# Optimization experiments

Measured on AMD Instinct MI355X. Metric: run time of the kernel, lower is better.

The kernel has to match this reference:

```python
import jax, jax.numpy as jnp
import numpy as np

B, N, D, H, L, K, V = 2, 2048, 512, 8, 4, 32, 256
HD = D // H
MOD = 4294967296.0
SCALE = 1.0 / np.sqrt(HD)


def _ln(x, g, b):
    m = x.mean(-1, keepdims=True)
    v = ((x - m) ** 2).mean(-1, keepdims=True)
    return (x - m) * jax.lax.rsqrt(v + 1e-5) * g + b


def _expmap0(v, c):
    sc = jnp.sqrt(c)
    vn = jnp.maximum(jnp.linalg.norm(v, axis=-1, keepdims=True), 1e-8)
    return jnp.tanh(sc * vn) * v / (sc * vn)


def _knn_poincare(pos, c):
    xx = jnp.sum(pos ** 2, -1)                                    # [N]
    d2 = jnp.maximum(xx[:, None] + xx[None, :] - 2.0 * pos @ pos.T, 0.0)
    denom = (1.0 - c * xx)[:, None] * (1.0 - c * xx)[None, :] + 1e-8
    arg = jnp.maximum(1.0 + 2.0 * c * d2 / denom, 1.0)
    dist = jnp.arccosh(arg) / jnp.sqrt(c)                         # [N,N]
    neg_d, idx = jax.lax.top_k(-dist, K)                          # smallest-k
    return -neg_d, idx                                            # [N,K],[N,K]


def _forward(hashes, indices, emb, hash_proj, Wb, bb, log_c, pos_tangent,
             Wq, bq, Wk, bk, Wv, bv, Wo, bo, W1, b1, W2, b2,
             g1, be1, g2, be2, log_tau, Wout, bout):
    c = jnp.exp(log_c)
    char = emb[indices]                                           # [B,N,D]
    he = (hashes[..., None].astype(jnp.float32) / MOD) @ hash_proj  # [B,N,D]
    x = jnp.concatenate([char, he], -1) @ Wb + bb                 # [B,N,D]

    # kNN structure computed under no_grad in the original
    pos = _expmap0(jax.lax.stop_gradient(pos_tangent), jax.lax.stop_gradient(c))
    attn_dists, idx = _knn_poincare(pos, jax.lax.stop_gradient(c))  # shared over batch

    for i in range(L):
        xn = _ln(x, g1[i], be1[i])
        q = (xn @ Wq[i] + bq[i]).reshape(B, N, H, HD).transpose(0, 2, 1, 3)
        k = (xn @ Wk[i] + bk[i]).reshape(B, N, H, HD).transpose(0, 2, 1, 3)
        v = (xn @ Wv[i] + bv[i]).reshape(B, N, H, HD).transpose(0, 2, 1, 3)
        kg = k[:, :, idx, :]                                      # [B,H,N,K,HD]
        vg = v[:, :, idx, :]
        fs = jnp.einsum('bhnd,bhnkd->bhnk', q, kg) * SCALE
        gs = -attn_dists[None, None] / (jnp.exp(log_tau[i]) + 1e-8)
        p = jax.nn.softmax(fs + gs, axis=-1)                      # [B,H,N,K]
        ao = jnp.einsum('bhnk,bhnkd->bhnd', p, vg)
        ao = ao.transpose(0, 2, 1, 3).reshape(B, N, D)
        x = x + ao @ Wo[i] + bo[i]
        xn2 = _ln(x, g2[i], be2[i])
        x = x + jax.nn.gelu(xn2 @ W1[i] + b1[i], approximate=False) @ W2[i] + b2[i]

    return x[:, -1, :] @ Wout + bout                              # [B,V]


def setup_inputs():
    key = jax.random.key(0)
    ks = jax.random.split(key, 20)
    rn = lambda k, s, sc=0.02: jax.random.normal(k, s, jnp.float32) * sc
    z = lambda s: jnp.zeros(s, jnp.float32)
    o = lambda s: jnp.ones(s, jnp.float32)
    return {
        'hashes': jax.random.randint(ks[0], (B, N), 0, 1000000),
        'indices': jax.random.randint(ks[1], (B, N), 0, V),
        'emb': rn(ks[2], (V, D)),
        'hash_proj': rn(ks[3], (1, D)),
        'Wb': rn(ks[4], (2 * D, D)),
        'bb': z((D,)),
        'log_c': jnp.array(0.0, jnp.float32),
        'pos_tangent': rn(ks[5], (N, D)),
        'Wq': rn(ks[6], (L, D, D)), 'bq': z((L, D)),
        'Wk': rn(ks[7], (L, D, D)), 'bk': z((L, D)),
        'Wv': rn(ks[8], (L, D, D)), 'bv': z((L, D)),
        'Wo': rn(ks[9], (L, D, D)), 'bo': z((L, D)),
        'W1': rn(ks[10], (L, D, 4 * D)), 'b1': z((L, 4 * D)),
        'W2': rn(ks[11], (L, 4 * D, D)), 'b2': z((L, D)),
        'g1': o((L, D)), 'be1': z((L, D)),
        'g2': o((L, D)), 'be2': z((L, D)),
        'log_tau': z((L,)),
        'Wout': rn(ks[12], (D, V)), 'bout': z((V,)),
    }


def reference(hashes, indices, emb, hash_proj, Wb, bb, log_c, pos_tangent,
              Wq, bq, Wk, bk, Wv, bv, Wo, bo, W1, b1, W2, b2,
              g1, be1, g2, be2, log_tau, Wout, bout):
    return _forward(hashes, indices, emb, hash_proj, Wb, bb, log_c, pos_tangent,
                    Wq, bq, Wk, bk, Wv, bv, Wo, bo, W1, b1, W2, b2,
                    g1, be1, g2, be2, log_tau, Wout, bout)
```

## Files before the change

### kernel.cpp

```cpp
#include <hip/hip_runtime.h>
#include <hip/hip_bf16.h>
#include <math.h>

#define Bb 2
#define Nn 2048
#define Dd 512
#define Hh 8
#define Ll 4
#define Kk 32
#define Vv 256
#define HDh 64
#define Mrows (Bb*Nn)

static constexpr float SCALE_QK = 0.125f;
static constexpr float INV_MOD = 1.0f / 4294967296.0f;

typedef _Float16 f16;
typedef _Float16 f16x8 __attribute__((ext_vector_type(8)));
typedef _Float16 f16x4 __attribute__((ext_vector_type(4)));
typedef _Float16 f16x2 __attribute__((ext_vector_type(2)));
typedef float f32x4 __attribute__((ext_vector_type(4)));
typedef unsigned long long u64;

__global__ void scal_kernel(const float* __restrict__ log_c,
                            const float* __restrict__ log_tau,
                            float* __restrict__ scal) {
    int t = threadIdx.x;
    if (t == 0) {
        float c = expf(log_c[0]);
        scal[0] = c;
        scal[1] = sqrtf(c);
    }
    if (t < Ll) scal[2 + t] = 1.0f / (expf(log_tau[t]) + 1e-8f);
}

__global__ __launch_bounds__(256)
void hvec_part_kernel(const float* __restrict__ hash_proj,
                      const float* __restrict__ Wb,
                      float* __restrict__ part) {
    const int b = blockIdx.x;
    const int t = threadIdx.x;
    float a0 = 0.f, a1 = 0.f;
#pragma unroll
    for (int i = 0; i < 16; i++) {
        int kx = b * 16 + i;
        float hp = hash_proj[kx];
        const float* wr = Wb + (size_t)(Dd + kx) * Dd;
        a0 = fmaf(hp, wr[t], a0);
        a1 = fmaf(hp, wr[t + 256], a1);
    }
    part[b * Dd + t]       = a0;
    part[b * Dd + t + 256] = a1;
}
__global__ __launch_bounds__(256)
void hvec_red_kernel(const float* __restrict__ part, float* __restrict__ hvec) {
    const int n = blockIdx.x * 256 + threadIdx.x;
    float acc = 0.f;
#pragma unroll
    for (int b = 0; b < 32; b++) acc += part[b * Dd + n];
    hvec[n] = acc;
}

__global__ void conv_kernel(const float* __restrict__ src, f16* __restrict__ dst, int n) {
    int i = blockIdx.x * 256 + threadIdx.x;
    if (i < n) dst[i] = (f16)src[i];
}

__global__ void pack_bias_kernel(const float* __restrict__ bq, const float* __restrict__ bk,
                                 const float* __restrict__ bv, float* __restrict__ bqkv) {
    int t = blockIdx.x * 256 + threadIdx.x;
    int l = t / 1536, r = t % 1536;
    const float* src = (r < 512) ? bq : ((r < 1024) ? bk : bv);
    bqkv[t] = src[l * 512 + (r & 511)];
}

__global__ __launch_bounds__(256)
void trans_kernel(const float* __restrict__ src, f16* __restrict__ dst,
                  int K, int N, long sStride, long dStride) {
    __shared__ float tile[32][33];
    const float* s = src + blockIdx.z * sStride;
    f16* d = dst + blockIdx.z * dStride;
    int k0 = blockIdx.y * 32, n0 = blockIdx.x * 32;
    int tx = threadIdx.x & 31, ty = threadIdx.x >> 5;
#pragma unroll
    for (int i = 0; i < 32; i += 8)
        tile[ty + i][tx] = s[(long)(k0 + ty + i) * N + n0 + tx];
    __syncthreads();
#pragma unroll
    for (int i = 0; i < 32; i += 8)
        d[(long)(n0 + ty + i) * K + k0 + tx] = (f16)tile[tx][ty + i];
}

__global__ __launch_bounds__(256)
void trans4_kernel(const float* __restrict__ Wq, const float* __restrict__ Wk,
                   const float* __restrict__ Wv, const float* __restrict__ Wo,
                   f16* __restrict__ Wqkvt, f16* __restrict__ Wot) {
    __shared__ float tile[32][33];
    const int which = blockIdx.z >> 2, l = blockIdx.z & 3;
    const float* s;
    f16* d;
    switch (which) {
        case 0: s = Wq + (size_t)l * 262144; d = Wqkvt + (size_t)l * 786432;          break;
        case 1: s = Wk + (size_t)l * 262144; d = Wqkvt + (size_t)l * 786432 + 262144; break;
        case 2: s = Wv + (size_t)l * 262144; d = Wqkvt + (size_t)l * 786432 + 524288; break;
        default:s = Wo + (size_t)l * 262144; d = Wot   + (size_t)l * 262144;          break;
    }
    int k0 = blockIdx.y * 32, n0 = blockIdx.x * 32;
    int tx = threadIdx.x & 31, ty = threadIdx.x >> 5;
#pragma unroll
    for (int i = 0; i < 32; i += 8)
        tile[ty + i][tx] = s[(long)(k0 + ty + i) * 512 + n0 + tx];
    __syncthreads();
#pragma unroll
    for (int i = 0; i < 32; i += 8)
        d[(long)(n0 + ty + i) * 512 + k0 + tx] = (f16)tile[tx][ty + i];
}

template<int TN, bool GATHER, bool RANK1, bool GELU, bool RES, bool OUT16>
__global__ __launch_bounds__(256)
void mgemm(const f16* __restrict__ A, const f16* __restrict__ Wt,
           const float* __restrict__ bias,
           const int* __restrict__ gidx,
           const int* __restrict__ hashes, const float* __restrict__ hvec,
           const float* __restrict__ resid,
           void* __restrict__ Cout, int M, int N, int K) {
    constexpr int TM  = 64;
    constexpr int WRN = (TN == 64) ? 2 : 1;
    constexpr int WCN = 4 / WRN;
    constexpr int WRE = TM / WRN;
    constexpr int NIT = WRE / 16;
    constexpr int ACH = TM * 8;
    constexpr int BCH = TN * 8;
    constexpr int NCH = ACH + BCH;
    constexpr int NCHT = NCH / 256;
    __shared__ __align__(16) f16 sm[NCH * 8];
    const int t = threadIdx.x;
    const int lane = t & 63;
    const int w = t >> 6;
    const int wr = w / WCN, wc = w % WCN;
    const int i0 = blockIdx.y * TM, j0 = blockIdx.x * TN;

    const f16* gsrc[NCHT];
#pragma unroll
    for (int q = 0; q < NCHT; q++) {
        int c = t + q * 256;
        if (c < ACH) {
            int m = c >> 3, kb = (c & 7) ^ (m & 7);
            long row = GATHER ? (long)gidx[i0 + m] : (long)(i0 + m);
            gsrc[q] = A + row * K + kb * 8;
        } else {
            int cc = c - ACH;
            int n = cc >> 3, kb = (cc & 7) ^ (n & 7);
            gsrc[q] = Wt + (long)(j0 + n) * K + kb * 8;
        }
    }

    f32x4 acc[NIT][2];
#pragma unroll
    for (int i = 0; i < NIT; i++)
#pragma unroll
        for (int j = 0; j < 2; j++) acc[i][j] = (f32x4){0.f, 0.f, 0.f, 0.f};

    for (int kt = 0; kt < K; kt += 64) {
        f16x8 stg[NCHT];
#pragma unroll
        for (int q = 0; q < NCHT; q++) stg[q] = *(const f16x8*)(gsrc[q] + kt);
        __syncthreads();
#pragma unroll
        for (int q = 0; q < NCHT; q++)
            *(f16x8*)(sm + (t + q * 256) * 8) = stg[q];
        __syncthreads();

#pragma unroll
        for (int kh = 0; kh < 2; kh++) {
            f16x8 af[NIT], bf[2];
#pragma unroll
            for (int i = 0; i < NIT; i++) {
                int m = wr * WRE + i * 16 + (lane & 15);
                int sl = m * 8 + ((kh * 4 + (lane >> 4)) ^ (m & 7));
                af[i] = *(const f16x8*)(sm + sl * 8);
            }
#pragma unroll
            for (int j = 0; j < 2; j++) {
                int n = wc * 32 + j * 16 + (lane & 15);
                int sl = ACH + n * 8 + ((kh * 4 + (lane >> 4)) ^ (n & 7));
                bf[j] = *(const f16x8*)(sm + sl * 8);
            }
#pragma unroll
            for (int i = 0; i < NIT; i++)
#pragma unroll
                for (int j = 0; j < 2; j++)
                    acc[i][j] = __builtin_amdgcn_mfma_f32_16x16x32_f16(af[i], bf[j], acc[i][j], 0, 0, 0);
        }
    }

    float* Cf = (float*)Cout;
    f16*   Ch = (f16*)Cout;
#pragma unroll
    for (int i = 0; i < NIT; i++) {
        int rbase = i0 + wr * WRE + i * 16 + ((lane >> 4) << 2);
#pragma unroll
        for (int v = 0; v < 4; v++) {
            int row = rbase + v;
            float hterm = RANK1 ? (float)hashes[row] * INV_MOD : 0.f;
#pragma unroll
            for (int j = 0; j < 2; j++) {
                int col = j0 + wc * 32 + j * 16 + (lane & 15);
                float val = acc[i][j][v] + bias[col];
                if (RANK1) val += hterm * hvec[col];
                if (GELU)  val = 0.5f * val * (1.f + erff(val * 0.7071067811865475f));
                if (RES)   val += resid[(long)row * N + col];
                if (OUT16) Ch[(long)row * N + col] = (f16)val;
                else       Cf[(long)row * N + col] = val;
            }
        }
    }
}

__global__ __launch_bounds__(256)
void mdist_kernel(const f16* __restrict__ poshl, const float* __restrict__ xx,
                  const float* __restrict__ scal, float* __restrict__ dist) {
    constexpr int TM = 64, TN = 64;
    constexpr int ACH = TM * 8, BCH = TN * 8, NCH = ACH + BCH;
    constexpr int NCHT = NCH / 256;
    constexpr int KK = 1024;
    __shared__ __align__(16) f16 sm[NCH * 8];
    const int t = threadIdx.x;
    const int lane = t & 63;
    const int w = t >> 6;
    const int wr = w >> 1, wc = w & 1;
    const int i0 = blockIdx.y * TM, j0 = blockIdx.x * TN;

    const f16* gsrc[NCHT];
#pragma unroll
    for (int q = 0; q < NCHT; q++) {
        int c = t + q * 256;
        if (c < ACH) {
            int m = c >> 3, kb = (c & 7) ^ (m & 7);
            gsrc[q] = poshl + (long)(i0 + m) * KK + kb * 8;
        } else {
            int cc = c - ACH;
            int n = cc >> 3, kb = (cc & 7) ^ (n & 7);
            gsrc[q] = poshl + (long)(j0 + n) * KK + kb * 8;
        }
    }

    f32x4 acc[2][2];
#pragma unroll
    for (int i = 0; i < 2; i++)
#pragma unroll
        for (int j = 0; j < 2; j++) acc[i][j] = (f32x4){0.f, 0.f, 0.f, 0.f};

    for (int kt = 0; kt < KK; kt += 64) {
        f16x8 stg[NCHT];
#pragma unroll
        for (int q = 0; q < NCHT; q++) stg[q] = *(const f16x8*)(gsrc[q] + kt);
        __syncthreads();
#pragma unroll
        for (int q = 0; q < NCHT; q++)
            *(f16x8*)(sm + (t + q * 256) * 8) = stg[q];
        __syncthreads();

#pragma unroll
        for (int kh = 0; kh < 2; kh++) {
            f16x8 af[2], bf[2];
#pragma unroll
            for (int i = 0; i < 2; i++) {
                int m = wr * 32 + i * 16 + (lane & 15);
                int sl = m * 8 + ((kh * 4 + (lane >> 4)) ^ (m & 7));
                af[i] = *(const f16x8*)(sm + sl * 8);
            }
#pragma unroll
            for (int j = 0; j < 2; j++) {
                int n = wc * 32 + j * 16 + (lane & 15);
                int sl = ACH + n * 8 + ((kh * 4 + (lane >> 4)) ^ (n & 7));
                bf[j] = *(const f16x8*)(sm + sl * 8);
            }
#pragma unroll
            for (int i = 0; i < 2; i++)
#pragma unroll
                for (int j = 0; j < 2; j++)
                    acc[i][j] = __builtin_amdgcn_mfma_f32_16x16x32_f16(af[i], bf[j], acc[i][j], 0, 0, 0);
        }
    }

    const float c = scal[0];
#pragma unroll
    for (int i = 0; i < 2; i++) {
        int rbase = i0 + wr * 32 + i * 16 + ((lane >> 4) << 2);
#pragma unroll
        for (int v = 0; v < 4; v++) {
            int row = rbase + v;
            float xi = xx[row];
#pragma unroll
            for (int j = 0; j < 2; j++) {
                int col = j0 + wc * 32 + j * 16 + (lane & 15);
                float xj = xx[col];
                float d2 = fmaxf(xi + xj - 2.f * acc[i][j][v], 0.f);
                float denom = (1.f - c * xi) * (1.f - c * xj) + 1e-8f;
                float arg = fmaxf(1.f + 2.f * c * d2 / denom, 1.f);
                dist[(long)row * Nn + col] = arg;
            }
        }
    }
}

__global__ __launch_bounds__(64)
void ln_kernel(const float* __restrict__ x, const float* __restrict__ g,
               const float* __restrict__ be, f16* __restrict__ xn) {
    const int row = blockIdx.x, t = threadIdx.x;
    const float4* xr = (const float4*)(x + (size_t)row * Dd);
    float4 v0 = xr[t], v1 = xr[t + 64];
    float s = v0.x + v0.y + v0.z + v0.w + v1.x + v1.y + v1.z + v1.w;
#pragma unroll
    for (int off = 32; off; off >>= 1) s += __shfl_xor(s, off, 64);
    float mean = s * (1.f / Dd);
    float d0x = v0.x - mean, d0y = v0.y - mean, d0z = v0.z - mean, d0w = v0.w - mean;
    float d1x = v1.x - mean, d1y = v1.y - mean, d1z = v1.z - mean, d1w = v1.w - mean;
    float q = d0x*d0x + d0y*d0y + d0z*d0z + d0w*d0w
            + d1x*d1x + d1y*d1y + d1z*d1z + d1w*d1w;
#pragma unroll
    for (int off = 32; off; off >>= 1) q += __shfl_xor(q, off, 64);
    float rstd = rsqrtf(q * (1.f / Dd) + 1e-5f);
    float4 g0 = ((const float4*)g)[t], g1v = ((const float4*)g)[t + 64];
    float4 b0 = ((const float4*)be)[t], b1v = ((const float4*)be)[t + 64];
    f16* xo = xn + (size_t)row * Dd;
    f16x4 o0, o1;
    o0[0] = (f16)(d0x * rstd * g0.x + b0.x);
    o0[1] = (f16)(d0y * rstd * g0.y + b0.y);
    o0[2] = (f16)(d0z * rstd * g0.z + b0.z);
    o0[3] = (f16)(d0w * rstd * g0.w + b0.w);
    o1[0] = (f16)(d1x * rstd * g1v.x + b1v.x);
    o1[1] = (f16)(d1y * rstd * g1v.y + b1v.y);
    o1[2] = (f16)(d1z * rstd * g1v.z + b1v.z);
    o1[3] = (f16)(d1w * rstd * g1v.w + b1v.w);
    *(f16x4*)(xo + t * 4)         = o0;
    *(f16x4*)(xo + (t + 64) * 4)  = o1;
}

__global__ __launch_bounds__(256)
void expmap_kernel(const float* __restrict__ vt, const float* __restrict__ scal,
                   f16* __restrict__ poshl, float* __restrict__ xx) {
    __shared__ float red[256];
    const int row = blockIdx.x, t = threadIdx.x;
    const float* vr = vt + (size_t)row * Dd;
    float v0 = vr[t], v1 = vr[t + 256];
    red[t] = v0 * v0 + v1 * v1;
    __syncthreads();
    for (int off = 128; off; off >>= 1) {
        if (t < off) red[t] += red[t + off];
        __syncthreads();
    }
    float total = red[0];
    float vn = fmaxf(sqrtf(total), 1e-8f);
    float sc = scal[1];
    float factor = tanhf(sc * vn) / (sc * vn);
    float p0 = factor * v0, p1 = factor * v1;
    f16 h0 = (f16)p0, h1 = (f16)p1;
    f16* pr = poshl + (size_t)row * 1024;
    pr[t]             = h0;
    pr[t + 256]       = h1;
    pr[512 + t]       = (f16)(p0 - (float)h0);
    pr[512 + t + 256] = (f16)(p1 - (float)h1);
    if (t == 0) xx[row] = factor * factor * total;
}

__global__ __launch_bounds__(256)
void topk_kernel(const float* __restrict__ dist, const float* __restrict__ scal,
                 float* __restrict__ outd, int* __restrict__ outi) {
    __shared__ unsigned wred[4];
    __shared__ unsigned bc;
    __shared__ __align__(8) u64 buf[128];
    const int t = threadIdx.x;
    const int w = t >> 6;
    const int n = blockIdx.x;
    const float sqc = scal[1];
    const uint4* dr = (const uint4*)(dist + (size_t)n * Nn);

    uint4 va = dr[t * 2];
    uint4 vb = dr[t * 2 + 1];
    unsigned k[8] = {va.x, va.y, va.z, va.w, vb.x, vb.y, vb.z, vb.w};
    const int g0 = t * 8;

    unsigned lo = 0x3F800000u;
    unsigned hi = 0x7F800001u;
    unsigned chi = 2048u;
    while (chi > 96u && (hi - lo) > 1u) {
        unsigned mid = lo + ((hi - lo) >> 1);
        int c = 0;
#pragma unroll
        for (int j = 0; j < 8; j++) c += (k[j] < mid) ? 1 : 0;
#pragma unroll
        for (int off = 32; off; off >>= 1) c += __shfl_xor(c, off, 64);
        __syncthreads();
        if ((t & 63) == 0) wred[w] = (unsigned)c;
        __syncthreads();
        unsigned ct = wred[0] + wred[1] + wred[2] + wred[3];
        if (ct >= 32u) { hi = mid; chi = ct; } else { lo = mid; }
    }

    if (chi <= 96u) {
        if (t == 0) bc = 0u;
        __syncthreads();
#pragma unroll
        for (int j = 0; j < 8; j++) {
            if (k[j] < hi) {
                unsigned s = atomicAdd(&bc, 1u);
                buf[s] = ((u64)k[j] << 11) | (u64)(unsigned)(g0 + j);
            }
        }
        __syncthreads();
        const int m = (int)chi;
        if (t < m) {
            u64 my = buf[t];
            int r = 0;
            for (int j = 0; j < m; j++) r += (buf[j] < my) ? 1 : 0;
            if (r < Kk) {
                float v = __uint_as_float((unsigned)(my >> 11));
                outd[n * Kk + r] = acoshf(v) / sqc;
                outi[n * Kk + r] = (int)(my & 2047u);
            }
        }
    } else {
        int c = 0;
#pragma unroll
        for (int j = 0; j < 8; j++) c += (k[j] < lo) ? 1 : 0;
#pragma unroll
        for (int off = 32; off; off >>= 1) c += __shfl_xor(c, off, 64);
        __syncthreads();
        if ((t & 63) == 0) wred[w] = (unsigned)c;
        if (t == 0) bc = 0u;
        __syncthreads();
        const int cless = (int)(wred[0] + wred[1] + wred[2] + wred[3]);
#pragma unroll
        for (int j = 0; j < 8; j++) {
            if (k[j] < lo) {
                unsigned s = atomicAdd(&bc, 1u);
                buf[s] = ((u64)k[j] << 11) | (u64)(unsigned)(g0 + j);
            }
        }
        __syncthreads();
        if (t < cless) {
            u64 my = buf[t];
            int r = 0;
            for (int j = 0; j < cless; j++) r += (buf[j] < my) ? 1 : 0;
            float v = __uint_as_float((unsigned)(my >> 11));
            outd[n * Kk + r] = acoshf(v) / sqc;
            outi[n * Kk + r] = (int)(my & 2047u);
        }
        const int need = Kk - cless;
        unsigned eqm = 0u;
#pragma unroll
        for (int j = 0; j < 8; j++) if (k[j] == lo) eqm |= (1u << j);
        const float dv = acoshf(__uint_as_float(lo)) / sqc;
        for (int s = 0; s < need; s++) {
            int mi = 0x7FFFFFFF;
#pragma unroll
            for (int j = 0; j < 8; j++)
                if (eqm & (1u << j)) mi = min(mi, g0 + j);
#pragma unroll
            for (int off = 32; off; off >>= 1) mi = min(mi, __shfl_xor(mi, off, 64));
            __syncthreads();
            if ((t & 63) == 0) wred[w] = (unsigned)mi;
            __syncthreads();
            int m4 = (int)min(min(wred[0], wred[1]), min(wred[2], wred[3]));
            int j = m4 - g0;
            if (j >= 0 && j < 8 && (eqm & (1u << j))) {
                eqm &= ~(1u << j);
                outd[n * Kk + cless + s] = dv;
                outi[n * Kk + cless + s] = m4;
            }
        }
    }
}

#define KVSTR 520
__global__ __launch_bounds__(256)
void attn_kernel(const f16* __restrict__ qkv, const float* __restrict__ adist,
                 const int* __restrict__ aidx, const float* __restrict__ scal,
                 int layer, f16* __restrict__ ao) {
    __shared__ __align__(16) f16 kv[64 * KVSTR];
    __shared__ __align__(16) f16 qs[512];
    __shared__ float ps[Hh][Kk];
    __shared__ float sdist[Kk];
    __shared__ int   sidx[Kk];
    const int t = threadIdx.x;
    const int b = blockIdx.x >> 11, n = blockIdx.x & (Nn - 1);
    const float inv_tau = scal[2 + layer];

    if (t < Kk) {
        sidx[t]  = aidx[n * Kk + t];
        sdist[t] = adist[n * Kk + t];
    }
    __syncthreads();

    {
        const size_t qrow = (size_t)(b * Nn + n) * 1536;
#pragma unroll
        for (int q = 0; q < 16; q++) {
            int c = q * 256 + t;
            int j = c >> 7, ci = c & 127;
            size_t src = (size_t)(b * Nn + sidx[j]) * 1536 + 512 + ci * 8;
            int dst = (ci < 64) ? (j * KVSTR + ci * 8)
                                : ((32 + j) * KVSTR + (ci - 64) * 8);
            *(f16x8*)(kv + dst) = *(const f16x8*)(qkv + src);
        }
        if (t < 64) *(f16x8*)(qs + t * 8) = *(const f16x8*)(qkv + qrow + t * 8);
    }
    __syncthreads();

    const int h = t >> 5, j = t & 31;
    float dot = 0.f;
#pragma unroll
    for (int i = 0; i < 8; i++) {
        f16x8 qa = *(const f16x8*)(qs + h * HDh + i * 8);
        f16x8 ka = *(const f16x8*)(kv + j * KVSTR + h * HDh + i * 8);
#pragma unroll
        for (int m = 0; m < 4; m++) {
            f16x2 qp = {qa[2 * m], qa[2 * m + 1]};
            f16x2 kp = {ka[2 * m], ka[2 * m + 1]};
            dot = __builtin_amdgcn_fdot2(qp, kp, dot, false);
        }
    }
    float s = dot * SCALE_QK - sdist[j] * inv_tau;
    float mx = s;
#pragma unroll
    for (int off = 16; off; off >>= 1) mx = fmaxf(mx, __shfl_xor(mx, off, 64));
    float e = expf(s - mx);
    float sum = e;
#pragma unroll
    for (int off = 16; off; off >>= 1) sum += __shfl_xor(sum, off, 64);
    ps[h][j] = e / sum;
    __syncthreads();

    const int d2 = t & 31;
    float a0 = 0.f, a1 = 0.f;
#pragma unroll
    for (int jj = 0; jj < Kk; jj++) {
        float p = ps[h][jj];
        f16x2 vv = *(const f16x2*)(kv + (32 + jj) * KVSTR + h * HDh + d2 * 2);
        a0 = fmaf(p, (float)vv[0], a0);
        a1 = fmaf(p, (float)vv[1], a1);
    }
    f16x2 outv; outv[0] = (f16)a0; outv[1] = (f16)a1;
    *(f16x2*)(ao + (size_t)(b * Nn + n) * Dd + h * HDh + d2 * 2) = outv;
}

__global__ void out_kernel(const float* __restrict__ x, const float* __restrict__ Wout,
                           const float* __restrict__ bout, float* __restrict__ out) {
    const int b = blockIdx.x, vc = threadIdx.x;
    const float* xr = x + ((size_t)(b * Nn + (Nn - 1))) * Dd;
    float acc = bout[vc];
    for (int d = 0; d < Dd; d++) acc = fmaf(xr[d], Wout[(size_t)d * Vv + vc], acc);
    out[b * Vv + vc] = acc;
}

static constexpr size_t X_OFF     = 0;
static constexpr size_t XN16_OFF  = 8388608;
static constexpr size_t QKV16_OFF = 12582912;
static constexpr size_t AO16_OFF  = 25165824;
static constexpr size_t H1_OFF    = 29360128;
static constexpr size_t AD_OFF    = 46137344;
static constexpr size_t AI_OFF    = 46399488;
static constexpr size_t SC_OFF    = 46661632;
static constexpr size_t HV_OFF    = 46661888;
static constexpr size_t XX_OFF    = 46663936;
static constexpr size_t BQKV_OFF  = 46672128;
static constexpr size_t EMB16_OFF = 46704896;
static constexpr size_t WBT_OFF   = 46967040;
static constexpr size_t WQKVT_OFF = 47491328;
static constexpr size_t WOT_OFF   = 53782784;
static constexpr size_t W1T_OFF   = 55879936;
static constexpr size_t W2T_OFF   = 64268544;
static constexpr size_t HP_OFF    = 72657152;

extern "C" void kernel_launch(void* const* d_in, const int* in_sizes, int n_in,
                              void* d_out, int out_size, void* d_ws, size_t ws_size,
                              hipStream_t stream) {
    (void)in_sizes; (void)n_in; (void)out_size; (void)ws_size;
    const int*   hashes    = (const int*)  d_in[0];
    const int*   indices   = (const int*)  d_in[1];
    const float* emb       = (const float*)d_in[2];
    const float* hash_proj = (const float*)d_in[3];
    const float* Wb        = (const float*)d_in[4];
    const float* bb        = (const float*)d_in[5];
    const float* log_c     = (const float*)d_in[6];
    const float* pos_t     = (const float*)d_in[7];
    const float* Wq        = (const float*)d_in[8];
    const float* bq        = (const float*)d_in[9];
    const float* Wk        = (const float*)d_in[10];
    const float* bk        = (const float*)d_in[11];
    const float* Wv        = (const float*)d_in[12];
    const float* bv        = (const float*)d_in[13];
    const float* Wo        = (const float*)d_in[14];
    const float* bo        = (const float*)d_in[15];
    const float* W1        = (const float*)d_in[16];
    const float* b1        = (const float*)d_in[17];
    const float* W2        = (const float*)d_in[18];
    const float* b2        = (const float*)d_in[19];
    const float* g1        = (const float*)d_in[20];
    const float* be1       = (const float*)d_in[21];
    const float* g2        = (const float*)d_in[22];
    const float* be2       = (const float*)d_in[23];
    const float* log_tau   = (const float*)d_in[24];
    const float* Wout      = (const float*)d_in[25];
    const float* bout      = (const float*)d_in[26];

    char* ws = (char*)d_ws;
    float* x      = (float*)(ws + X_OFF);
    f16*   xn16   = (f16*)  (ws + XN16_OFF);
    f16*   qkv16  = (f16*)  (ws + QKV16_OFF);
    f16*   ao16   = (f16*)  (ws + AO16_OFF);
    f16*   h1     = (f16*)  (ws + H1_OFF);
    float* adist  = (float*)(ws + AD_OFF);
    int*   aidx   = (int*)  (ws + AI_OFF);
    float* scal   = (float*)(ws + SC_OFF);
    float* hvec   = (float*)(ws + HV_OFF);
    float* xxb    = (float*)(ws + XX_OFF);
    float* bqkv   = (float*)(ws + BQKV_OFF);
    f16*   emb16  = (f16*)  (ws + EMB16_OFF);
    f16*   Wbt    = (f16*)  (ws + WBT_OFF);
    f16*   Wqkvt  = (f16*)  (ws + WQKVT_OFF);
    f16*   Wot    = (f16*)  (ws + WOT_OFF);
    f16*   W1t    = (f16*)  (ws + W1T_OFF);
    f16*   W2t    = (f16*)  (ws + W2T_OFF);
    float* hpart  = (float*)(ws + HP_OFF);
    f16*   poshl  = (f16*)  (ws + AO16_OFF);
    float* distb  = (float*)(ws + H1_OFF);

    scal_kernel<<<1, 64, 0, stream>>>(log_c, log_tau, scal);
    hvec_part_kernel<<<32, 256, 0, stream>>>(hash_proj, Wb, hpart);
    hvec_red_kernel<<<2, 256, 0, stream>>>(hpart, hvec);
    pack_bias_kernel<<<24, 256, 0, stream>>>(bq, bk, bv, bqkv);
    conv_kernel<<<(Vv * Dd + 255) / 256, 256, 0, stream>>>(emb, emb16, Vv * Dd);
    trans_kernel<<<dim3(16, 16, 1), 256, 0, stream>>>(Wb, Wbt, 512, 512, 0, 0);
    trans4_kernel<<<dim3(16, 16, 16), 256, 0, stream>>>(Wq, Wk, Wv, Wo, Wqkvt, Wot);
    trans_kernel<<<dim3(64, 16, Ll), 256, 0, stream>>>(W1, W1t, 512, 2048, 1048576, 1048576);
    trans_kernel<<<dim3(16, 64, Ll), 256, 0, stream>>>(W2, W2t, 2048, 512, 1048576, 1048576);

    mgemm<64, true, true, false, false, false><<<dim3(8, 64), 256, 0, stream>>>(
        emb16, Wbt, bb, indices, hashes, hvec, nullptr, x, Mrows, Dd, Dd);

    expmap_kernel<<<Nn, 256, 0, stream>>>(pos_t, scal, poshl, xxb);
    mdist_kernel<<<dim3(32, 32), 256, 0, stream>>>(poshl, xxb, scal, distb);
    topk_kernel<<<Nn, 256, 0, stream>>>(distb, scal, adist, aidx);

    for (int l = 0; l < Ll; l++) {
        ln_kernel<<<Mrows, 64, 0, stream>>>(x, g1 + l * Dd, be1 + l * Dd, xn16);
        mgemm<128, false, false, false, false, true><<<dim3(12, 64), 256, 0, stream>>>(
            xn16, Wqkvt + (size_t)l * 786432, bqkv + l * 1536,
            nullptr, nullptr, nullptr, nullptr, qkv16, Mrows, 1536, Dd);
        attn_kernel<<<Bb * Nn, 256, 0, stream>>>(qkv16, adist, aidx, scal, l, ao16);
        mgemm<64, false, false, false, true, false><<<dim3(8, 64), 256, 0, stream>>>(
            ao16, Wot + (size_t)l * 262144, bo + l * Dd,
            nullptr, nullptr, nullptr, x, x, Mrows, Dd, Dd);
        ln_kernel<<<Mrows, 64, 0, stream>>>(x, g2 + l * Dd, be2 + l * Dd, xn16);
        mgemm<128, false, false, true, false, true><<<dim3(16, 64), 256, 0, stream>>>(
            xn16, W1t + (size_t)l * 1048576, b1 + l * 4 * Dd,
            nullptr, nullptr, nullptr, nullptr, h1, Mrows, 4 * Dd, Dd);
        mgemm<64, false, false, false, true, false><<<dim3(8, 64), 256, 0, stream>>>(
            h1, W2t + (size_t)l * 1048576, b2 + l * Dd,
            nullptr, nullptr, nullptr, x, x, Mrows, Dd, 4 * Dd);
    }

    out_kernel<<<Bb, Vv, 0, stream>>>(x, Wout, bout, (float*)d_out);
}
```

Before: 639.2 us.

## Double-buffer GEMM tiles with direct global-to-LDS async loads

Replaces the register-staged load/store of A and W tiles in the generic GEMM and the distance GEMM with global_load_lds direct-to-LDS copies into a two-slot shared buffer. The next K-tile is prefetched while MFMAs run on the current one, removing one barrier per iteration and the register staging. This doubles LDS use per block, which may lower occupancy. Correctness depends on the vmcnt wait and the barrier ordering, and on the per-lane LDS destination layout matching what global_load_lds actually writes.

```diff
diff --git a/kernel.cpp b/kernel.cpp
--- a/kernel.cpp
+++ b/kernel.cpp
@@ -21,6 +21,12 @@
 typedef _Float16 f16x2 __attribute__((ext_vector_type(2)));
 typedef float f32x4 __attribute__((ext_vector_type(4)));
 typedef unsigned long long u64;
+
+#define AS_GLOBAL(p) ((const __attribute__((address_space(1))) void*)(p))
+#define AS_LDS(p)    ((__attribute__((address_space(3))) void*)(p))
+__device__ __forceinline__ void gload16(const f16* g, f16* l) {
+    __builtin_amdgcn_global_load_lds(AS_GLOBAL(g), AS_LDS(l), 16, 0, 0);
+}
 
 __global__ void scal_kernel(const float* __restrict__ log_c,
                             const float* __restrict__ log_tau,
@@ -133,7 +139,7 @@
     constexpr int BCH = TN * 8;
     constexpr int NCH = ACH + BCH;
     constexpr int NCHT = NCH / 256;
-    __shared__ __align__(16) f16 sm[NCH * 8];
+    __shared__ __align__(16) f16 sm[2][NCH * 8];
     const int t = threadIdx.x;
     const int lane = t & 63;
     const int w = t >> 6;
@@ -161,16 +167,18 @@
 #pragma unroll
         for (int j = 0; j < 2; j++) acc[i][j] = (f32x4){0.f, 0.f, 0.f, 0.f};
 
-    for (int kt = 0; kt < K; kt += 64) {
-        f16x8 stg[NCHT];
-#pragma unroll
-        for (int q = 0; q < NCHT; q++) stg[q] = *(const f16x8*)(gsrc[q] + kt);
-        __syncthreads();
-#pragma unroll
-        for (int q = 0; q < NCHT; q++)
-            *(f16x8*)(sm + (t + q * 256) * 8) = stg[q];
-        __syncthreads();
-
+#pragma unroll
+    for (int q = 0; q < NCHT; q++)
+        gload16(gsrc[q], &sm[0][(t + q * 256) * 8]);
+
+    auto step = [&](int kt, const f16* rbuf, f16* wbuf) {
+        asm volatile("s_waitcnt vmcnt(0)" ::: "memory");
+        __syncthreads();
+        if (kt + 64 < K) {
+#pragma unroll
+            for (int q = 0; q < NCHT; q++)
+                gload16(gsrc[q] + kt + 64, wbuf + (t + q * 256) * 8);
+        }
 #pragma unroll
         for (int kh = 0; kh < 2; kh++) {
             f16x8 af[NIT], bf[2];
@@ -178,13 +186,13 @@
             for (int i = 0; i < NIT; i++) {
                 int m = wr * WRE + i * 16 + (lane & 15);
                 int sl = m * 8 + ((kh * 4 + (lane >> 4)) ^ (m & 7));
-                af[i] = *(const f16x8*)(sm + sl * 8);
+                af[i] = *(const f16x8*)(rbuf + sl * 8);
             }
 #pragma unroll
             for (int j = 0; j < 2; j++) {
                 int n = wc * 32 + j * 16 + (lane & 15);
                 int sl = ACH + n * 8 + ((kh * 4 + (lane >> 4)) ^ (n & 7));
-                bf[j] = *(const f16x8*)(sm + sl * 8);
+                bf[j] = *(const f16x8*)(rbuf + sl * 8);
             }
 #pragma unroll
             for (int i = 0; i < NIT; i++)
@@ -192,6 +200,11 @@
                 for (int j = 0; j < 2; j++)
                     acc[i][j] = __builtin_amdgcn_mfma_f32_16x16x32_f16(af[i], bf[j], acc[i][j], 0, 0, 0);
         }
+    };
+
+    for (int kt = 0; kt < K; kt += 128) {
+        step(kt,      sm[0], sm[1]);
+        step(kt + 64, sm[1], sm[0]);
     }
 
     float* Cf = (float*)Cout;
@@ -224,7 +237,7 @@
     constexpr int ACH = TM * 8, BCH = TN * 8, NCH = ACH + BCH;
     constexpr int NCHT = NCH / 256;
     constexpr int KK = 1024;
-    __shared__ __align__(16) f16 sm[NCH * 8];
+    __shared__ __align__(16) f16 sm[2][NCH * 8];
     const int t = threadIdx.x;
     const int lane = t & 63;
     const int w = t >> 6;
@@ -251,16 +264,18 @@
 #pragma unroll
         for (int j = 0; j < 2; j++) acc[i][j] = (f32x4){0.f, 0.f, 0.f, 0.f};
 
-    for (int kt = 0; kt < KK; kt += 64) {
-        f16x8 stg[NCHT];
-#pragma unroll
-        for (int q = 0; q < NCHT; q++) stg[q] = *(const f16x8*)(gsrc[q] + kt);
-        __syncthreads();
-#pragma unroll
-        for (int q = 0; q < NCHT; q++)
-            *(f16x8*)(sm + (t + q * 256) * 8) = stg[q];
-        __syncthreads();
-
+#pragma unroll
+    for (int q = 0; q < NCHT; q++)
+        gload16(gsrc[q], &sm[0][(t + q * 256) * 8]);
+
+    auto step = [&](int kt, const f16* rbuf, f16* wbuf) {
+        asm volatile("s_waitcnt vmcnt(0)" ::: "memory");
+        __syncthreads();
+        if (kt + 64 < KK) {
+#pragma unroll
+            for (int q = 0; q < NCHT; q++)
+                gload16(gsrc[q] + kt + 64, wbuf + (t + q * 256) * 8);
+        }
 #pragma unroll
         for (int kh = 0; kh < 2; kh++) {
             f16x8 af[2], bf[2];
@@ -268,13 +283,13 @@
             for (int i = 0; i < 2; i++) {
                 int m = wr * 32 + i * 16 + (lane & 15);
                 int sl = m * 8 + ((kh * 4 + (lane >> 4)) ^ (m & 7));
-                af[i] = *(const f16x8*)(sm + sl * 8);
+                af[i] = *(const f16x8*)(rbuf + sl * 8);
             }
 #pragma unroll
             for (int j = 0; j < 2; j++) {
                 int n = wc * 32 + j * 16 + (lane & 15);
                 int sl = ACH + n * 8 + ((kh * 4 + (lane >> 4)) ^ (n & 7));
-                bf[j] = *(const f16x8*)(sm + sl * 8);
+                bf[j] = *(const f16x8*)(rbuf + sl * 8);
             }
 #pragma unroll
             for (int i = 0; i < 2; i++)
@@ -282,6 +297,11 @@
                 for (int j = 0; j < 2; j++)
                     acc[i][j] = __builtin_amdgcn_mfma_f32_16x16x32_f16(af[i], bf[j], acc[i][j], 0, 0, 0);
         }
+    };
+
+    for (int kt = 0; kt < KK; kt += 128) {
+        step(kt,      sm[0], sm[1]);
+        step(kt + 64, sm[1], sm[0]);
     }
 
     const float c = scal[0];
```

After: 627.8 us. Within noise of the previous version (-1.8%).
